# Kernel tuning notes

Measured on AMD Instinct MI355X. Metric: run time of the kernel, lower is better.

## Reference

```python
import jax, jax.numpy as jnp
import numpy as np

B, C, H, W = 16, 512, 64, 64


def setup_inputs() -> dict:
    key = jax.random.key(0)
    ks = jax.random.split(key, 5)
    s = 0.02  # init scale for projection weights
    return {
        "x": jax.random.normal(ks[0], (B, C, H, W), jnp.float32),
        "Wqkv": jax.random.normal(ks[1], (3 * C, C), jnp.float32) * s,
        "bqkv": jnp.zeros((3 * C,), jnp.float32),
        "Wm": jax.random.normal(ks[2], (2 * C, C), jnp.float32) * s,
        "bm": jnp.zeros((2 * C,), jnp.float32),
        "Wg": jax.random.normal(ks[3], (C, 2 * C), jnp.float32) * s,
        "bg": jnp.zeros((C,), jnp.float32),
        "Wr": jax.random.normal(ks[4], (C, C), jnp.float32) * s,
        "br": jnp.zeros((C,), jnp.float32),
    }


def reference(x, Wqkv, bqkv, Wm, bm, Wg, bg, Wr, br):
    b, c, h, w = x.shape
    n = h * w
    xf = x.reshape(b, c, n)  # [B,C,N]
    # qkv projection: [B,3C,N] -> q,k,v each [B,C,N]
    qkv = jnp.einsum('oc,bcn->bon', Wqkv, xf) + bqkv[None, :, None]
    q, k, v = qkv[:, :c], qkv[:, c:2 * c], qkv[:, 2 * c:]
    # modulation from v: mq, mk each [B,C,N]
    mqk = jnp.einsum('oc,bcn->bon', Wm, v) + bm[None, :, None]
    mq, mk = mqk[:, :c], mqk[:, c:]
    _q = jax.nn.softmax(-jax.nn.relu(q * mq), axis=-1)   # softmax over N
    _k = jax.nn.relu(k * mk)                             # [B,C,N]
    # channel attention: [B,C,N] @ [B,N,C] -> [B,C,C]
    scores = jnp.einsum('bcn,bdn->bcd', _q, _k) / jnp.sqrt(jnp.float32(c))
    attn = jax.nn.softmax(scores, axis=-1)
    y = jnp.einsum('bcd,bdn->bcn', attn, v)              # [B,C,N]
    y2d = y.reshape(b, c, h, w)
    # gated residual: g = sigmoid(W_g @ cat(y, x))
    catf = jnp.concatenate([y, xf], axis=1)              # [B,2C,N]
    g = jax.nn.sigmoid(jnp.einsum('oc,bcn->bon', Wg, catf) + bg[None, :, None]).reshape(b, c, h, w)
    r = (jnp.einsum('oc,bcn->bon', Wr, xf) + br[None, :, None]).reshape(b, c, h, w)
    out = g * r + (1.0 - g) * y2d
    return (out, attn)
```

## Files before the change

### kernel.cpp

```cpp
#include <hip/hip_runtime.h>
#include <math.h>

#define Bb 16
#define Cc 512
#define Nn 4096
#define CN (512L * 4096)

typedef __bf16 bf16x8 __attribute__((ext_vector_type(8)));
typedef float  floatx4 __attribute__((ext_vector_type(4)));

__device__ __forceinline__ unsigned short f2bf(float f) {
    unsigned int u = __float_as_uint(f);
    unsigned int r = (u + 0x7FFFu + ((u >> 16) & 1u)) >> 16;
    return (unsigned short)r;
}
__device__ __forceinline__ float bf2f(unsigned short s) {
    return __uint_as_float(((unsigned int)s) << 16);
}

__device__ __forceinline__ void gload16(const void* g, void* l) {
    __builtin_amdgcn_global_load_lds(
        (const __attribute__((address_space(1))) unsigned int*)g,
        (__attribute__((address_space(3))) unsigned int*)l,
        16, 0, 0);
}

template<int OUTF32, int SPLIT>
__global__ __launch_bounds__(256) void gemm_bt(
    const unsigned short* __restrict__ A1,
    const unsigned short* __restrict__ A2, int lda, int asplit,
    const unsigned short* __restrict__ B, int ldb,
    const float* __restrict__ bias,
    void* __restrict__ Cv, int ldc,
    int K, float scale,
    long sA, long sB, long sC)
{
    __shared__ __align__(16) unsigned short Alds[3][8 * 512];
    __shared__ __align__(16) unsigned short Blds[3][8 * 512];

    const int nwg  = gridDim.x * gridDim.y * gridDim.z;
    const int orig = blockIdx.x + gridDim.x * (blockIdx.y + gridDim.y * blockIdx.z);
    const int q8   = nwg >> 3, r8 = nwg & 7;
    const int xcd  = orig & 7, sub_i = orig >> 3;
    const int logical = (xcd < r8 ? xcd * (q8 + 1) : r8 * (q8 + 1) + (xcd - r8) * q8) + sub_i;
    const int bx = logical % gridDim.x;
    const int btmp = logical / gridDim.x;
    const int by = btmp % gridDim.y;
    const int bz = btmp / gridDim.y;

    const int t    = threadIdx.x;
    const int lane = t & 63;
    const int wave = t >> 6;
    const int m0 = by * 128;
    const int n0 = bx * 128;
    const int wm = (wave >> 1) * 64;
    const int wn = (wave & 1) * 64;

    const unsigned short* Ab1 = A1 + (size_t)bz * sA;
    const unsigned short* Ab2 = SPLIT ? (A2 + (size_t)bz * sA) : nullptr;
    const unsigned short* Bb_ = B + (size_t)bz * sB;

    const int srow = lane & 15;
    const int sk   = (lane >> 4) * 8;
    const int sub0 = wave * 2;

    const unsigned short* gA0 = Ab1 + (size_t)(m0 + (sub0    ) * 16 + srow) * lda + sk;
    const unsigned short* gA1 = Ab1 + (size_t)(m0 + (sub0 + 1) * 16 + srow) * lda + sk;
    const unsigned short* gB0 = Bb_ + (size_t)(n0 + (sub0    ) * 16 + srow) * ldb + sk;
    const unsigned short* gB1 = Bb_ + (size_t)(n0 + (sub0 + 1) * 16 + srow) * ldb + sk;
    const ptrdiff_t sjump = SPLIT ? (Ab2 - Ab1) - (ptrdiff_t)asplit : 0;

    auto stage = [&](int buf, int k0) {
        const unsigned short* a0 = gA0 + k0;
        const unsigned short* a1 = gA1 + k0;
        if (SPLIT && k0 >= asplit) { a0 += sjump; a1 += sjump; }
        gload16(a0,       &Alds[buf][(sub0    ) * 512]);
        gload16(gB0 + k0, &Blds[buf][(sub0    ) * 512]);
        gload16(a1,       &Alds[buf][(sub0 + 1) * 512]);
        gload16(gB1 + k0, &Blds[buf][(sub0 + 1) * 512]);
    };

    floatx4 acc[4][4] = {};

    const int nt = K >> 5;
    stage(0, 0);
    if (nt > 1) stage(1, 32);
    int cur = 0;

    for (int ti = 0; ti < nt; ++ti) {
        if (ti + 2 < nt) {
            int bufn = cur + 2; if (bufn >= 3) bufn -= 3;
            stage(bufn, (ti + 2) << 5);
            asm volatile("s_waitcnt vmcnt(8)" ::: "memory");
        } else if (ti + 1 < nt) {
            asm volatile("s_waitcnt vmcnt(4)" ::: "memory");
        } else {
            asm volatile("s_waitcnt vmcnt(0)" ::: "memory");
        }
        __builtin_amdgcn_s_barrier();
        __builtin_amdgcn_sched_barrier(0);

        bf16x8 af[4], bfr[4];
#pragma unroll
        for (int i = 0; i < 4; ++i) {
            af[i]  = *(const bf16x8*)&Alds[cur][((wm >> 4) + i) * 512 + lane * 8];
            bfr[i] = *(const bf16x8*)&Blds[cur][((wn >> 4) + i) * 512 + lane * 8];
        }
        __builtin_amdgcn_s_setprio(1);
#pragma unroll
        for (int i = 0; i < 4; ++i)
#pragma unroll
            for (int j = 0; j < 4; ++j)
                acc[i][j] = __builtin_amdgcn_mfma_f32_16x16x32_bf16(af[i], bfr[j], acc[i][j], 0, 0, 0);
        __builtin_amdgcn_s_setprio(0);

        asm volatile("s_waitcnt lgkmcnt(0)" ::: "memory");
        __builtin_amdgcn_s_barrier();
        __builtin_amdgcn_sched_barrier(0);
        cur = (cur == 2) ? 0 : cur + 1;
    }

    const int rbase = (lane >> 4) * 4;
    const int cofs  = lane & 15;
#pragma unroll
    for (int j = 0; j < 4; ++j) {
        int col = n0 + wn + j * 16 + cofs;
        float bv = bias ? bias[col] : 0.0f;
#pragma unroll
        for (int i = 0; i < 4; ++i) {
#pragma unroll
            for (int r = 0; r < 4; ++r) {
                int row = m0 + wm + i * 16 + rbase + r;
                float v = acc[i][j][r] * scale + bv;
                if (OUTF32) {
                    float* C = (float*)Cv + (size_t)bz * sC;
                    C[(size_t)row * ldc + col] = v;
                } else {
                    unsigned short* C = (unsigned short*)Cv + (size_t)bz * sC;
                    C[(size_t)row * ldc + col] = f2bf(v);
                }
            }
        }
    }
}

__global__ __launch_bounds__(256) void wcast(const float* __restrict__ w,
                                             unsigned short* __restrict__ o, int n)
{
    int i = (blockIdx.x * 256 + threadIdx.x) * 4;
    float4 v = *(const float4*)&w[i];
    ushort4 u;
    u.x = f2bf(v.x); u.y = f2bf(v.y); u.z = f2bf(v.z); u.w = f2bf(v.w);
    *(ushort4*)&o[i] = u;
}

__global__ __launch_bounds__(256) void transpose_x(const float* __restrict__ x,
                                                   unsigned short* __restrict__ xp)
{
    __shared__ unsigned short tile[64][65];
    const float* X = x + (size_t)blockIdx.z * CN;
    unsigned short* O = xp + (size_t)blockIdx.z * CN;
    int n0 = blockIdx.x * 64, c0 = blockIdx.y * 64;
    int tq = (threadIdx.x & 15) * 4, tr = threadIdx.x >> 4;
#pragma unroll
    for (int r = 0; r < 4; ++r) {
        int cl = tr + r * 16;
        float4 v = *(const float4*)&X[(size_t)(c0 + cl) * 4096 + n0 + tq];
        tile[tq + 0][cl] = f2bf(v.x);
        tile[tq + 1][cl] = f2bf(v.y);
        tile[tq + 2][cl] = f2bf(v.z);
        tile[tq + 3][cl] = f2bf(v.w);
    }
    __syncthreads();
#pragma unroll
    for (int r = 0; r < 4; ++r) {
        int nl = tr + r * 16;
        ushort4 o;
        o.x = tile[nl][tq + 0]; o.y = tile[nl][tq + 1];
        o.z = tile[nl][tq + 2]; o.w = tile[nl][tq + 3];
        *(ushort4*)&O[(size_t)(n0 + nl) * 512 + c0 + tq] = o;
    }
}

__global__ __launch_bounds__(256) void qk_transform(
    const unsigned short* __restrict__ qkv, const unsigned short* __restrict__ mqk,
    unsigned short* __restrict__ T, int coff, int neg)
{
    __shared__ __align__(8) unsigned short tile[64][68];
    const unsigned short* S1 = qkv + (size_t)blockIdx.z * (4096L * 1536) + coff;
    const unsigned short* S2 = mqk + (size_t)blockIdx.z * (4096L * 1024) + coff;
    unsigned short* O = T + (size_t)blockIdx.z * CN;
    int n0 = blockIdx.x * 64, c0 = blockIdx.y * 64;
    int tq = (threadIdx.x & 15) * 4, tr = threadIdx.x >> 4;
#pragma unroll
    for (int r = 0; r < 4; ++r) {
        int nl = tr + r * 16;
        ushort4 a = *(const ushort4*)&S1[(size_t)(n0 + nl) * 1536 + c0 + tq];
        ushort4 m = *(const ushort4*)&S2[(size_t)(n0 + nl) * 1024 + c0 + tq];
        float f0 = fmaxf(bf2f(a.x) * bf2f(m.x), 0.0f);
        float f1 = fmaxf(bf2f(a.y) * bf2f(m.y), 0.0f);
        float f2 = fmaxf(bf2f(a.z) * bf2f(m.z), 0.0f);
        float f3 = fmaxf(bf2f(a.w) * bf2f(m.w), 0.0f);
        if (neg) { f0 = -f0; f1 = -f1; f2 = -f2; f3 = -f3; }
        ushort4 p;
        p.x = f2bf(f0); p.y = f2bf(f1); p.z = f2bf(f2); p.w = f2bf(f3);
        *(ushort4*)&tile[nl][tq] = p;
    }
    __syncthreads();
#pragma unroll
    for (int r = 0; r < 4; ++r) {
        int cl = tr + r * 16;
        ushort4 o;
        o.x = tile[tq + 0][cl]; o.y = tile[tq + 1][cl];
        o.z = tile[tq + 2][cl]; o.w = tile[tq + 3][cl];
        *(ushort4*)&O[(size_t)(c0 + cl) * 4096 + n0 + tq] = o;
    }
}

__global__ __launch_bounds__(256) void qsoftmax_bf(unsigned short* __restrict__ Q)
{
    unsigned short* p = Q + (size_t)blockIdx.x * 4096;
    const int t = threadIdx.x;
    const int lane = t & 63;
    const int wv = t >> 6;
    __shared__ float red[8];

    float vals[16];
    float mx = -1e30f;
#pragma unroll
    for (int i = 0; i < 16; ++i) {
        float v = bf2f(p[t + i * 256]);
        vals[i] = v;
        mx = fmaxf(mx, v);
    }
#pragma unroll
    for (int off = 32; off > 0; off >>= 1) mx = fmaxf(mx, __shfl_xor(mx, off));
    if (lane == 0) red[wv] = mx;
    __syncthreads();
    mx = fmaxf(fmaxf(red[0], red[1]), fmaxf(red[2], red[3]));

    float sum = 0.0f;
#pragma unroll
    for (int i = 0; i < 16; ++i) {
        vals[i] = __expf(vals[i] - mx);
        sum += vals[i];
    }
#pragma unroll
    for (int off = 32; off > 0; off >>= 1) sum += __shfl_xor(sum, off);
    if (lane == 0) red[4 + wv] = sum;
    __syncthreads();
    sum = red[4] + red[5] + red[6] + red[7];
    float inv = 1.0f / sum;
#pragma unroll
    for (int i = 0; i < 16; ++i) p[t + i * 256] = f2bf(vals[i] * inv);
}

__global__ __launch_bounds__(256) void attn_softmax_dual(
    float* __restrict__ attnf, unsigned short* __restrict__ attnb)
{
    float* p = attnf + (size_t)blockIdx.x * 512;
    unsigned short* pb = attnb + (size_t)blockIdx.x * 512;
    const int t = threadIdx.x;
    const int lane = t & 63;
    const int wv = t >> 6;
    __shared__ float red[8];

    float v0 = p[t], v1 = p[t + 256];
    float mx = fmaxf(v0, v1);
#pragma unroll
    for (int off = 32; off > 0; off >>= 1) mx = fmaxf(mx, __shfl_xor(mx, off));
    if (lane == 0) red[wv] = mx;
    __syncthreads();
    mx = fmaxf(fmaxf(red[0], red[1]), fmaxf(red[2], red[3]));

    float e0 = __expf(v0 - mx);
    float e1 = __expf(v1 - mx);
    float sum = e0 + e1;
#pragma unroll
    for (int off = 32; off > 0; off >>= 1) sum += __shfl_xor(sum, off);
    if (lane == 0) red[4 + wv] = sum;
    __syncthreads();
    sum = red[4] + red[5] + red[6] + red[7];
    float inv = 1.0f / sum;
    float a0 = e0 * inv, a1 = e1 * inv;
    p[t] = a0;        p[t + 256] = a1;
    pb[t] = f2bf(a0); pb[t + 256] = f2bf(a1);
}

__global__ __launch_bounds__(256) void final_fuse(
    const unsigned short* __restrict__ gl, const unsigned short* __restrict__ rr,
    const unsigned short* __restrict__ yy, float* __restrict__ out)
{
    __shared__ __align__(16) float tile[64][68];
    size_t bo = (size_t)blockIdx.z * CN;
    const unsigned short* G_ = gl + bo;
    const unsigned short* R_ = rr + bo;
    const unsigned short* Y_ = yy + bo;
    float* O = out + bo;
    int n0 = blockIdx.x * 64, c0 = blockIdx.y * 64;
    int tq = (threadIdx.x & 15) * 4, tr = threadIdx.x >> 4;
#pragma unroll
    for (int r = 0; r < 4; ++r) {
        int nl = tr + r * 16;
        size_t base = (size_t)(n0 + nl) * 512 + c0 + tq;
        ushort4 g4 = *(const ushort4*)&G_[base];
        ushort4 r4 = *(const ushort4*)&R_[base];
        ushort4 y4 = *(const ushort4*)&Y_[base];
        float4 o;
        float g;
        g = 1.0f / (1.0f + __expf(-bf2f(g4.x))); o.x = g * bf2f(r4.x) + (1.0f - g) * bf2f(y4.x);
        g = 1.0f / (1.0f + __expf(-bf2f(g4.y))); o.y = g * bf2f(r4.y) + (1.0f - g) * bf2f(y4.y);
        g = 1.0f / (1.0f + __expf(-bf2f(g4.z))); o.z = g * bf2f(r4.z) + (1.0f - g) * bf2f(y4.z);
        g = 1.0f / (1.0f + __expf(-bf2f(g4.w))); o.w = g * bf2f(r4.w) + (1.0f - g) * bf2f(y4.w);
        *(float4*)&tile[nl][tq] = o;
    }
    __syncthreads();
#pragma unroll
    for (int r = 0; r < 4; ++r) {
        int cl = tr + r * 16;
        float4 o;
        o.x = tile[tq + 0][cl]; o.y = tile[tq + 1][cl];
        o.z = tile[tq + 2][cl]; o.w = tile[tq + 3][cl];
        *(float4*)&O[(size_t)(c0 + cl) * 4096 + n0 + tq] = o;
    }
}

extern "C" void kernel_launch(void* const* d_in, const int* in_sizes, int n_in,
                              void* d_out, int out_size, void* d_ws, size_t ws_size,
                              hipStream_t stream)
{
    const float* x    = (const float*)d_in[0];
    const float* Wqkv = (const float*)d_in[1];
    const float* bqkv = (const float*)d_in[2];
    const float* Wm   = (const float*)d_in[3];
    const float* bm   = (const float*)d_in[4];
    const float* Wg   = (const float*)d_in[5];
    const float* bg   = (const float*)d_in[6];
    const float* Wr   = (const float*)d_in[7];
    const float* br   = (const float*)d_in[8];

    float* out      = (float*)d_out;
    float* attn_all = out + (size_t)Bb * CN;

    unsigned short* wq_bf = (unsigned short*)d_ws;
    unsigned short* wm_bf = wq_bf + 1536 * 512;
    unsigned short* wg_bf = wm_bf + 1024 * 512;
    unsigned short* wr_bf = wg_bf + 512 * 1024;
    unsigned short* dyn   = wr_bf + 512 * 512;
    const size_t fixed_bytes = (size_t)(1536 * 512 + 1024 * 512 + 512 * 1024 + 512 * 512) * 2;
    const size_t per_batch_bytes = (size_t)4096 * 4096 * 2;

    int G = 16;
    while (G > 1 && fixed_bytes + (size_t)G * per_batch_bytes > ws_size) G >>= 1;

    dim3 blk(256);
    const float inv_sqrt_c = 0.044194173824159216f;

    wcast<<<1536 * 512 / 1024, blk, 0, stream>>>(Wqkv, wq_bf, 1536 * 512);
    wcast<<<1024 * 512 / 1024, blk, 0, stream>>>(Wm,   wm_bf, 1024 * 512);
    wcast<<<512 * 1024 / 1024, blk, 0, stream>>>(Wg,   wg_bf, 512 * 1024);
    wcast<<<512 * 512  / 1024, blk, 0, stream>>>(Wr,   wr_bf, 512 * 512);

    for (int b0 = 0; b0 < Bb; b0 += G) {
        unsigned short* xp   = dyn;
        unsigned short* qkvp = xp   + (size_t)G * 4096 * 512;
        unsigned short* mqkp = qkvp + (size_t)G * 4096 * 1536;
        unsigned short* qp   = mqkp + (size_t)G * 4096 * 1024;
        unsigned short* kp   = qp   + (size_t)G * CN;
        unsigned short* yp   = mqkp;
        unsigned short* glp  = mqkp + (size_t)G * CN;
        unsigned short* rp   = qp;
        unsigned short* abf  = kp;

        const float* xg   = x + (size_t)b0 * CN;
        float* outg       = out + (size_t)b0 * CN;
        float* attng      = attn_all + (size_t)b0 * 512 * 512;

        transpose_x<<<dim3(64, 8, G), blk, 0, stream>>>(xg, xp);

        gemm_bt<0, 0><<<dim3(12, 32, G), blk, 0, stream>>>(
            xp, nullptr, 512, 0, wq_bf, 512, bqkv, qkvp, 1536,
            512, 1.0f, 4096L * 512, 0L, 4096L * 1536);

        gemm_bt<0, 0><<<dim3(8, 32, G), blk, 0, stream>>>(
            qkvp + 1024, nullptr, 1536, 0, wm_bf, 512, bm, mqkp, 1024,
            512, 1.0f, 4096L * 1536, 0L, 4096L * 1024);

        qk_transform<<<dim3(64, 8, G), blk, 0, stream>>>(qkvp, mqkp, qp, 0, 1);
        qk_transform<<<dim3(64, 8, G), blk, 0, stream>>>(qkvp, mqkp, kp, 512, 0);

        qsoftmax_bf<<<G * 512, blk, 0, stream>>>(qp);

        gemm_bt<1, 0><<<dim3(4, 4, G), blk, 0, stream>>>(
            qp, nullptr, 4096, 0, kp, 4096, nullptr, attng, 512,
            4096, inv_sqrt_c, CN, CN, 512L * 512);

        attn_softmax_dual<<<G * 512, blk, 0, stream>>>(attng, abf);

        gemm_bt<0, 0><<<dim3(4, 32, G), blk, 0, stream>>>(
            qkvp + 1024, nullptr, 1536, 0, abf, 512, nullptr, yp, 512,
            512, 1.0f, 4096L * 1536, 512L * 512, 4096L * 512);

        gemm_bt<0, 1><<<dim3(4, 32, G), blk, 0, stream>>>(
            yp, xp, 512, 512, wg_bf, 1024, bg, glp, 512,
            1024, 1.0f, 4096L * 512, 0L, 4096L * 512);

        gemm_bt<0, 0><<<dim3(4, 32, G), blk, 0, stream>>>(
            xp, nullptr, 512, 0, wr_bf, 512, br, rp, 512,
            512, 1.0f, 4096L * 512, 0L, 4096L * 512);

        final_fuse<<<dim3(64, 8, G), blk, 0, stream>>>(glp, rp, yp, outg);
    }
}
```

Baseline: 1.230 ms.

## Add 256x256-tile 512-thread GEMM kernel for projection GEMMs

Adds a new bf16 MFMA GEMM kernel that uses 256x256 output tiles, 8 waves per block, 64-wide K steps and a double-buffered LDS pipeline. All projection and attention-apply GEMMs with N=4096 rows now use it instead of the 128x128 kernel. The larger tiles are meant to raise arithmetic intensity and cut redundant global loads. In exchange, each block uses more LDS and registers, occupancy is lower, and the grid is smaller. The XCD swizzle logic is factored into a shared helper.

```diff
diff --git a/kernel.cpp b/kernel.cpp
--- a/kernel.cpp
+++ b/kernel.cpp
@@ -23,6 +23,138 @@
         (const __attribute__((address_space(1))) unsigned int*)g,
         (__attribute__((address_space(3))) unsigned int*)l,
         16, 0, 0);
+}
+
+__device__ __forceinline__ void xcd_swizzle(int& bx, int& by, int& bz) {
+    const int nwg  = gridDim.x * gridDim.y * gridDim.z;
+    const int orig = blockIdx.x + gridDim.x * (blockIdx.y + gridDim.y * blockIdx.z);
+    const int q8   = nwg >> 3, r8 = nwg & 7;
+    const int xcd  = orig & 7, sub_i = orig >> 3;
+    const int logical = (xcd < r8 ? xcd * (q8 + 1) : r8 * (q8 + 1) + (xcd - r8) * q8) + sub_i;
+    bx = logical % gridDim.x;
+    const int btmp = logical / gridDim.x;
+    by = btmp % gridDim.y;
+    bz = btmp / gridDim.y;
+}
+
+template<int OUTF32, int SPLIT>
+__global__ __launch_bounds__(512) void gemm_bt256(
+    const unsigned short* __restrict__ A1,
+    const unsigned short* __restrict__ A2, int lda, int asplit,
+    const unsigned short* __restrict__ B, int ldb,
+    const float* __restrict__ bias,
+    void* __restrict__ Cv, int ldc,
+    int K, float scale,
+    long sA, long sB, long sC)
+{
+    __shared__ __align__(16) unsigned short Alds[2][32 * 512];
+    __shared__ __align__(16) unsigned short Blds[2][32 * 512];
+
+    int bx, by, bz;
+    xcd_swizzle(bx, by, bz);
+
+    const int t    = threadIdx.x;
+    const int lane = t & 63;
+    const int wave = t >> 6;
+    const int m0 = by * 256;
+    const int n0 = bx * 256;
+    const int wm = (wave >> 2) * 128;
+    const int wn = (wave & 3) * 64;
+
+    const unsigned short* Ab1 = A1 + (size_t)bz * sA;
+    const unsigned short* Ab2 = SPLIT ? (A2 + (size_t)bz * sA) : nullptr;
+    const unsigned short* Bb_ = B + (size_t)bz * sB;
+
+    const int srow = lane & 15;
+    const int sk8  = (lane >> 4) * 8;
+    const ptrdiff_t sjump = SPLIT ? (Ab2 - Ab1) - (ptrdiff_t)asplit : 0;
+
+    const unsigned short* gA[4];
+    const unsigned short* gB[4];
+#pragma unroll
+    for (int u = 0; u < 4; ++u) {
+        int si = wave * 4 + u;
+        int rowsub = si >> 1, kh = si & 1;
+        gA[u] = Ab1 + (size_t)(m0 + rowsub * 16 + srow) * lda + kh * 32 + sk8;
+        gB[u] = Bb_ + (size_t)(n0 + rowsub * 16 + srow) * ldb + kh * 32 + sk8;
+    }
+
+    auto stage = [&](int buf, int k0) {
+        const bool hi = SPLIT && (k0 >= asplit);
+#pragma unroll
+        for (int u = 0; u < 4; ++u) {
+            int si = wave * 4 + u;
+            const unsigned short* a = gA[u] + k0;
+            if (hi) a += sjump;
+            gload16(a,          &Alds[buf][si * 512]);
+            gload16(gB[u] + k0, &Blds[buf][si * 512]);
+        }
+    };
+
+    floatx4 acc[8][4] = {};
+
+    const int nt = K >> 6;
+    stage(0, 0);
+    int cur = 0;
+
+    for (int ti = 0; ti < nt; ++ti) {
+        if (ti + 1 < nt) {
+            stage(cur ^ 1, (ti + 1) << 6);
+            asm volatile("s_waitcnt vmcnt(8)" ::: "memory");
+        } else {
+            asm volatile("s_waitcnt vmcnt(0)" ::: "memory");
+        }
+        __builtin_amdgcn_s_barrier();
+        __builtin_amdgcn_sched_barrier(0);
+
+        const int ra = wm >> 4;
+        const int rb = wn >> 4;
+#pragma unroll
+        for (int s = 0; s < 2; ++s) {
+            bf16x8 af[8], bfr[4];
+#pragma unroll
+            for (int i = 0; i < 8; ++i)
+                af[i] = *(const bf16x8*)&Alds[cur][((ra + i) * 2 + s) * 512 + lane * 8];
+#pragma unroll
+            for (int j = 0; j < 4; ++j)
+                bfr[j] = *(const bf16x8*)&Blds[cur][((rb + j) * 2 + s) * 512 + lane * 8];
+            __builtin_amdgcn_s_setprio(1);
+#pragma unroll
+            for (int i = 0; i < 8; ++i)
+#pragma unroll
+                for (int j = 0; j < 4; ++j)
+                    acc[i][j] = __builtin_amdgcn_mfma_f32_16x16x32_bf16(af[i], bfr[j], acc[i][j], 0, 0, 0);
+            __builtin_amdgcn_s_setprio(0);
+        }
+
+        asm volatile("s_waitcnt lgkmcnt(0)" ::: "memory");
+        __builtin_amdgcn_s_barrier();
+        __builtin_amdgcn_sched_barrier(0);
+        cur ^= 1;
+    }
+
+    const int rbase = (lane >> 4) * 4;
+    const int cofs  = lane & 15;
+#pragma unroll
+    for (int j = 0; j < 4; ++j) {
+        int col = n0 + wn + j * 16 + cofs;
+        float bv = bias ? bias[col] : 0.0f;
+#pragma unroll
+        for (int i = 0; i < 8; ++i) {
+#pragma unroll
+            for (int r = 0; r < 4; ++r) {
+                int row = m0 + wm + i * 16 + rbase + r;
+                float v = acc[i][j][r] * scale + bv;
+                if (OUTF32) {
+                    float* C = (float*)Cv + (size_t)bz * sC;
+                    C[(size_t)row * ldc + col] = v;
+                } else {
+                    unsigned short* C = (unsigned short*)Cv + (size_t)bz * sC;
+                    C[(size_t)row * ldc + col] = f2bf(v);
+                }
+            }
+        }
+    }
 }
 
 template<int OUTF32, int SPLIT>
@@ -38,15 +170,8 @@
     __shared__ __align__(16) unsigned short Alds[3][8 * 512];
     __shared__ __align__(16) unsigned short Blds[3][8 * 512];
 
-    const int nwg  = gridDim.x * gridDim.y * gridDim.z;
-    const int orig = blockIdx.x + gridDim.x * (blockIdx.y + gridDim.y * blockIdx.z);
-    const int q8   = nwg >> 3, r8 = nwg & 7;
-    const int xcd  = orig & 7, sub_i = orig >> 3;
-    const int logical = (xcd < r8 ? xcd * (q8 + 1) : r8 * (q8 + 1) + (xcd - r8) * q8) + sub_i;
-    const int bx = logical % gridDim.x;
-    const int btmp = logical / gridDim.x;
-    const int by = btmp % gridDim.y;
-    const int bz = btmp / gridDim.y;
+    int bx, by, bz;
+    xcd_swizzle(bx, by, bz);
 
     const int t    = threadIdx.x;
     const int lane = t & 63;
@@ -354,6 +479,7 @@
     while (G > 1 && fixed_bytes + (size_t)G * per_batch_bytes > ws_size) G >>= 1;
 
     dim3 blk(256);
+    dim3 blk512(512);
     const float inv_sqrt_c = 0.044194173824159216f;
 
     wcast<<<1536 * 512 / 1024, blk, 0, stream>>>(Wqkv, wq_bf, 1536 * 512);
@@ -378,11 +504,11 @@
 
         transpose_x<<<dim3(64, 8, G), blk, 0, stream>>>(xg, xp);
 
-        gemm_bt<0, 0><<<dim3(12, 32, G), blk, 0, stream>>>(
+        gemm_bt256<0, 0><<<dim3(6, 16, G), blk512, 0, stream>>>(
             xp, nullptr, 512, 0, wq_bf, 512, bqkv, qkvp, 1536,
             512, 1.0f, 4096L * 512, 0L, 4096L * 1536);
 
-        gemm_bt<0, 0><<<dim3(8, 32, G), blk, 0, stream>>>(
+        gemm_bt256<0, 0><<<dim3(4, 16, G), blk512, 0, stream>>>(
             qkvp + 1024, nullptr, 1536, 0, wm_bf, 512, bm, mqkp, 1024,
             512, 1.0f, 4096L * 1536, 0L, 4096L * 1024);
 
@@ -397,15 +523,15 @@
 
         attn_softmax_dual<<<G * 512, blk, 0, stream>>>(attng, abf);
 
-        gemm_bt<0, 0><<<dim3(4, 32, G), blk, 0, stream>>>(
+        gemm_bt256<0, 0><<<dim3(2, 16, G), blk512, 0, stream>>>(
             qkvp + 1024, nullptr, 1536, 0, abf, 512, nullptr, yp, 512,
             512, 1.0f, 4096L * 1536, 512L * 512, 4096L * 512);
 
-        gemm_bt<0, 1><<<dim3(4, 32, G), blk, 0, stream>>>(
+        gemm_bt256<0, 1><<<dim3(2, 16, G), blk512, 0, stream>>>(
             yp, xp, 512, 512, wg_bf, 1024, bg, glp, 512,
             1024, 1.0f, 4096L * 512, 0L, 4096L * 512);
 
-        gemm_bt<0, 0><<<dim3(4, 32, G), blk, 0, stream>>>(
+        gemm_bt256<0, 0><<<dim3(2, 16, G), blk512, 0, stream>>>(
             xp, nullptr, 512, 0, wr_bf, 512, br, rp, 512,
             512, 1.0f, 4096L * 512, 0L, 4096L * 512);
 
```

After: 1.202 ms. 2.2% less time.
